# Kernel tuning notes

Measured on AMD Instinct MI355X. Metric: run time of the kernel, lower is better.

The kernel has to match this reference:

```python
import jax, jax.numpy as jnp
import numpy as np

H, W = 256, 832            # full-res organized point cloud (HEIGHT/WIDTH globals)
STRIDE_H, STRIDE_W = 2, 4  # stride_H_list[0], stride_W_list[0]
OUT_H, OUT_W = 128, 208    # out_H_list[0], out_W_list[0]
KH, KW = 12, 20            # layer0 kernel_size
K = 32                     # layer0 K_sample


def _sa_layer(pts, h_idx, w_idx, w1, b1, w2, b2, w3, b3):
    """PointNet SA: strided center selection, window KNN grouping, MLP, max-pool.
    pts: (B,H,W,3); h_idx/w_idx: (M,) full-res grid coords of selected centers.
    """
    B = pts.shape[0]
    pts_flat = pts.reshape(B, H * W, 3)
    center_idx = h_idx * W + w_idx                      # (M,)
    centers = pts_flat[:, center_idx]                   # (B,M,3)  fast_select gather
    # candidate window around each center (clipped at borders)
    dh = jnp.arange(KH) - KH // 2
    dw = jnp.arange(KW) - KW // 2
    cand_h = jnp.clip(h_idx[:, None] + dh, 0, H - 1)    # (M,KH)
    cand_w = jnp.clip(w_idx[:, None] + dw, 0, W - 1)    # (M,KW)
    cand_idx = (cand_h[:, :, None] * W + cand_w[:, None, :]).reshape(-1, KH * KW)  # (M,P)
    cand = pts_flat[:, cand_idx]                        # (B,M,P,3) irregular gather
    d2 = jnp.sum((cand - centers[:, :, None, :]) ** 2, axis=-1)  # (B,M,P)
    _, nn = jax.lax.top_k(-d2, K)                       # K nearest within window
    knn = jnp.take_along_axis(cand, nn[..., None], axis=2)       # (B,M,K,3)
    rel = knn - centers[:, :, None, :]                  # local coordinates
    h = jax.nn.relu(rel @ w1 + b1)                      # mlp [8,8,16]
    h = jax.nn.relu(h @ w2 + b2)
    h = jax.nn.relu(h @ w3 + b3)
    return centers, jnp.max(h, axis=2)                  # (B,M,3), (B,M,16)


def setup_inputs() -> dict:
    key = jax.random.key(0)
    ks = jax.random.split(key, 5)
    return {
        "pos1": jax.random.normal(ks[0], (2, H, W, 3), jnp.float32) * 5.0,
        "pos2": jax.random.normal(ks[1], (2, H, W, 3), jnp.float32) * 5.0,
        "w1": jax.random.normal(ks[2], (3, 8), jnp.float32) * 0.3,
        "b1": jnp.zeros((8,), jnp.float32),
        "w2": jax.random.normal(ks[3], (8, 8), jnp.float32) * 0.3,
        "b2": jnp.zeros((8,), jnp.float32),
        "w3": jax.random.normal(ks[4], (8, 16), jnp.float32) * 0.3,
        "b3": jnp.zeros((16,), jnp.float32),
    }


def reference(pos1, pos2, w1, b1, w2, b2, w3, b3):
    # get_selected_idx for level 0: strided grid subsampling
    h_idx = jnp.repeat(jnp.arange(OUT_H) * STRIDE_H, OUT_W)  # (M,)
    w_idx = jnp.tile(jnp.arange(OUT_W) * STRIDE_W, OUT_H)    # (M,)
    _, f1 = _sa_layer(pos1, h_idx, w_idx, w1, b1, w2, b2, w3, b3)
    _, f2 = _sa_layer(pos2, h_idx, w_idx, w1, b1, w2, b2, w3, b3)
    return jnp.concatenate([f1, f2], axis=-1)  # (B, OUT_H*OUT_W, 32)
```

## Files before the change

kernel.cpp:

```cpp
#include <hip/hip_runtime.h>
#include <hip/hip_bf16.h>

#define HH 256
#define WW 832
#define OHH 128
#define OWW 208
#define NCAND 240
#define MM (OHH*OWW)

__device__ __forceinline__ int iclamp(int v, int lo, int hi) { return min(max(v, lo), hi); }
__device__ __forceinline__ int mbcnt64(unsigned long long m) {
    return __builtin_amdgcn_mbcnt_hi((unsigned)(m >> 32),
           __builtin_amdgcn_mbcnt_lo((unsigned)(m & 0xFFFFFFFFull), 0));
}

__global__ void __launch_bounds__(256) sa_fused(
    const float* __restrict__ pos1, const float* __restrict__ pos2,
    const float* __restrict__ w1, const float* __restrict__ b1,
    const float* __restrict__ w2, const float* __restrict__ b2,
    const float* __restrict__ w3, const float* __restrict__ b3,
    float* __restrict__ out)
{
    __shared__ float4 sW1[8];
    __shared__ float4 sW2[8][2];
    __shared__ float4 sW3[16][2];
    __shared__ float  sB2v[8];
    __shared__ float  sB3v[16];
    __shared__ int    selJ[128];

    const int t = threadIdx.x;
    if (t < 8)  sW1[t] = make_float4(w1[t], w1[8 + t], w1[16 + t], b1[t]);
    if (t < 16) { int o = t >> 1, g = (t & 1) * 4;
        sW2[o][t & 1] = make_float4(w2[g*8 + o], w2[(g+1)*8 + o], w2[(g+2)*8 + o], w2[(g+3)*8 + o]); }
    if (t < 32) { int o = t >> 1, g = (t & 1) * 4;
        sW3[o][t & 1] = make_float4(w3[g*16 + o], w3[(g+1)*16 + o], w3[(g+2)*16 + o], w3[(g+3)*16 + o]); }
    if (t < 8)  sB2v[t] = b2[t];
    if (t < 16) sB3v[t] = b3[t];
    __syncthreads();

    const int lane = t & 63;
    const int wid  = t >> 6;
    const int m    = blockIdx.x * 4 + wid;
    const int b    = blockIdx.y & 1;
    const int cl   = blockIdx.y >> 1;
    const float* __restrict__ base = (cl ? pos2 : pos1) + (size_t)b * (HH * WW * 3);

    const unsigned um = (unsigned)m;
    const int oh = (int)(um / OWW);
    const int ow = (int)(um - (unsigned)oh * OWW);
    const int h0 = oh * 2, w0 = ow * 4;

    const float cx = base[(h0 * WW + w0) * 3 + 0];
    const float cy = base[(h0 * WW + w0) * 3 + 1];
    const float cz = base[(h0 * WW + w0) * 3 + 2];

    unsigned d2b[4];
    #pragma unroll
    for (int q = 0; q < 4; ++q) {
        int j  = q * 64 + lane;
        int kh = (j * 205) >> 12;
        int kw = j - kh * 20;
        int ch = iclamp(h0 - 6 + kh, 0, HH - 1);
        int cw = iclamp(w0 - 10 + kw, 0, WW - 1);
        const float* p = base + (ch * WW + cw) * 3;
        float dx = __fsub_rn(p[0], cx);
        float dy = __fsub_rn(p[1], cy);
        float dz = __fsub_rn(p[2], cz);
        float dd = __fadd_rn(__fadd_rn(__fmul_rn(dx, dx), __fmul_rn(dy, dy)), __fmul_rn(dz, dz));
        d2b[q] = (j < NCAND) ? __float_as_uint(dd) : 0xFFFFFFFFu;
    }

    unsigned T = 0;
    unsigned long long sm0 = 0, sm1 = 0, sm2 = 0, sm3 = 0;
    bool exact = false;
    for (int bpos = 30; bpos >= 0; --bpos) {
        unsigned Q = T | (1u << bpos);
        unsigned long long t0 = __ballot(d2b[0] < Q);
        unsigned long long t1 = __ballot(d2b[1] < Q);
        unsigned long long t2 = __ballot(d2b[2] < Q);
        unsigned long long t3 = __ballot(d2b[3] < Q);
        int c = __popcll(t0) + __popcll(t1) + __popcll(t2) + __popcll(t3);
        if (c == 32) { sm0 = t0; sm1 = t1; sm2 = t2; sm3 = t3; exact = true; break; }
        if (c < 32) T = Q;
    }
    if (!exact) {
        unsigned long long l0 = __ballot(d2b[0] < T);
        unsigned long long l1 = __ballot(d2b[1] < T);
        unsigned long long l2 = __ballot(d2b[2] < T);
        unsigned long long l3 = __ballot(d2b[3] < T);
        unsigned long long e0 = __ballot(d2b[0] == T);
        unsigned long long e1 = __ballot(d2b[1] == T);
        unsigned long long e2 = __ballot(d2b[2] == T);
        unsigned long long e3 = __ballot(d2b[3] == T);
        int c_lt = __popcll(l0) + __popcll(l1) + __popcll(l2) + __popcll(l3);
        int r = 32 - c_lt;
        int p1 = __popcll(e0), p2 = p1 + __popcll(e1), p3 = p2 + __popcll(e2);
        bool s0 = (d2b[0] < T) || ((d2b[0] == T) && (mbcnt64(e0) < r));
        bool s1 = (d2b[1] < T) || ((d2b[1] == T) && (p1 + mbcnt64(e1) < r));
        bool s2 = (d2b[2] < T) || ((d2b[2] == T) && (p2 + mbcnt64(e2) < r));
        bool s3 = (d2b[3] < T) || ((d2b[3] == T) && (p3 + mbcnt64(e3) < r));
        sm0 = __ballot(s0); sm1 = __ballot(s1); sm2 = __ballot(s2); sm3 = __ballot(s3);
    }

    {
        int b1 = __popcll(sm0);
        int b2 = b1 + __popcll(sm1);
        int b3 = b2 + __popcll(sm2);
        int lb = wid * 32;
        if ((sm0 >> lane) & 1) selJ[lb +      mbcnt64(sm0)] = lane;
        if ((sm1 >> lane) & 1) selJ[lb + b1 + mbcnt64(sm1)] = 64 + lane;
        if ((sm2 >> lane) & 1) selJ[lb + b2 + mbcnt64(sm2)] = 128 + lane;
        if ((sm3 >> lane) & 1) selJ[lb + b3 + mbcnt64(sm3)] = 192 + lane;
    }
    asm volatile("s_waitcnt lgkmcnt(0)" ::: "memory");
    __builtin_amdgcn_sched_barrier(0);

    {
        unsigned jj = (unsigned)selJ[wid * 32 + (lane & 31)];
        int kh = (int)((jj * 205u) >> 12);
        int kw = (int)jj - kh * 20;
        int ch = iclamp(h0 - 6 + kh, 0, HH - 1);
        int cw = iclamp(w0 - 10 + kw, 0, WW - 1);
        const float* p = base + (ch * WW + cw) * 3;
        float rx = __fsub_rn(p[0], cx);
        float ry = __fsub_rn(p[1], cy);
        float rz = __fsub_rn(p[2], cz);

        float h1[8];
        #pragma unroll
        for (int o = 0; o < 8; ++o) {
            float4 wv = sW1[o];
            h1[o] = fmaxf(fmaf(rz, wv.z, fmaf(ry, wv.y, fmaf(rx, wv.x, wv.w))), 0.f);
        }
        float h2[8];
        #pragma unroll
        for (int o = 0; o < 8; ++o) {
            float4 a = sW2[o][0], c4 = sW2[o][1];
            float v = sB2v[o];
            v = fmaf(h1[0], a.x, v);  v = fmaf(h1[1], a.y, v);
            v = fmaf(h1[2], a.z, v);  v = fmaf(h1[3], a.w, v);
            v = fmaf(h1[4], c4.x, v); v = fmaf(h1[5], c4.y, v);
            v = fmaf(h1[6], c4.z, v); v = fmaf(h1[7], c4.w, v);
            h2[o] = fmaxf(v, 0.f);
        }
        const int ob = (lane >> 5) << 3;
        float h3[8];
        #pragma unroll
        for (int o = 0; o < 8; ++o) {
            float4 a = sW3[ob + o][0], c4 = sW3[ob + o][1];
            float v = sB3v[ob + o];
            v = fmaf(h2[0], a.x, v);  v = fmaf(h2[1], a.y, v);
            v = fmaf(h2[2], a.z, v);  v = fmaf(h2[3], a.w, v);
            v = fmaf(h2[4], c4.x, v); v = fmaf(h2[5], c4.y, v);
            v = fmaf(h2[6], c4.z, v); v = fmaf(h2[7], c4.w, v);
            h3[o] = v;
        }
        #pragma unroll
        for (int o = 0; o < 8; ++o) {
            h3[o] = fmaxf(h3[o], __shfl_xor(h3[o], 16));
            h3[o] = fmaxf(h3[o], __shfl_xor(h3[o], 8));
            h3[o] = fmaxf(h3[o], __shfl_xor(h3[o], 4));
            h3[o] = fmaxf(h3[o], __shfl_xor(h3[o], 2));
            h3[o] = fmaxf(h3[o], __shfl_xor(h3[o], 1));
        }
        if ((lane & 31) == 0) {
            float4* dst = (float4*)(out + ((size_t)(b * MM + m) * 32) + (size_t)cl * 16 + ob);
            dst[0] = make_float4(fmaxf(h3[0], 0.f), fmaxf(h3[1], 0.f), fmaxf(h3[2], 0.f), fmaxf(h3[3], 0.f));
            dst[1] = make_float4(fmaxf(h3[4], 0.f), fmaxf(h3[5], 0.f), fmaxf(h3[6], 0.f), fmaxf(h3[7], 0.f));
        }
    }
}

extern "C" void kernel_launch(void* const* d_in, const int* in_sizes, int n_in,
                              void* d_out, int out_size, void* d_ws, size_t ws_size,
                              hipStream_t stream) {
    const float* pos1 = (const float*)d_in[0];
    const float* pos2 = (const float*)d_in[1];
    const float* w1   = (const float*)d_in[2];
    const float* b1   = (const float*)d_in[3];
    const float* w2   = (const float*)d_in[4];
    const float* b2   = (const float*)d_in[5];
    const float* w3   = (const float*)d_in[6];
    const float* b3   = (const float*)d_in[7];
    float* out = (float*)d_out;

    dim3 grid(MM / 4, 4);
    sa_fused<<<grid, 256, 0, stream>>>(pos1, pos2, w1, b1, w2, b2, w3, b3, out);
}
```

Baseline: 94.87 us.

## Stash selected relative coords in LDS and use packed FMA for MLP

The selected neighbours' relative xyz, already computed during the distance pass, are now written to shared memory. This replaces the index list that forced a second irregular global gather and index decode. The MLP layers are rewritten to use two-wide vector FMAs (packed fp32) with weights stored in pairs. The cost is more registers to hold dx/dy/dz for all candidates, and wider LDS writes (float4 instead of int).

New measurement: 95.53 us. About the same (+0.7%).

```diff
diff --git a/kernel.cpp b/kernel.cpp
--- a/kernel.cpp
+++ b/kernel.cpp
@@ -7,6 +7,8 @@
 #define OWW 208
 #define NCAND 240
 #define MM (OHH*OWW)
+
+typedef float v2f __attribute__((ext_vector_type(2)));
 
 __device__ __forceinline__ int iclamp(int v, int lo, int hi) { return min(max(v, lo), hi); }
 __device__ __forceinline__ int mbcnt64(unsigned long long m) {
@@ -21,21 +23,22 @@
     const float* __restrict__ w3, const float* __restrict__ b3,
     float* __restrict__ out)
 {
-    __shared__ float4 sW1[8];
-    __shared__ float4 sW2[8][2];
-    __shared__ float4 sW3[16][2];
-    __shared__ float  sB2v[8];
-    __shared__ float  sB3v[16];
-    __shared__ int    selJ[128];
+    __shared__ v2f sW1p[3][4];
+    __shared__ v2f sW2p[8][4];
+    __shared__ v2f sW3p[8][8];
+    __shared__ v2f sB1p[4], sB2p[4], sB3p[8];
+    __shared__ float4 selRel[128];
 
     const int t = threadIdx.x;
-    if (t < 8)  sW1[t] = make_float4(w1[t], w1[8 + t], w1[16 + t], b1[t]);
-    if (t < 16) { int o = t >> 1, g = (t & 1) * 4;
-        sW2[o][t & 1] = make_float4(w2[g*8 + o], w2[(g+1)*8 + o], w2[(g+2)*8 + o], w2[(g+3)*8 + o]); }
-    if (t < 32) { int o = t >> 1, g = (t & 1) * 4;
-        sW3[o][t & 1] = make_float4(w3[g*16 + o], w3[(g+1)*16 + o], w3[(g+2)*16 + o], w3[(g+3)*16 + o]); }
-    if (t < 8)  sB2v[t] = b2[t];
-    if (t < 16) sB3v[t] = b3[t];
+    if (t < 12)              { int i = t >> 2,  op = t & 3;
+        sW1p[i][op] = (v2f){w1[i*8 + 2*op], w1[i*8 + 2*op + 1]}; }
+    if (t >= 16 && t < 48)   { int u = t - 16, i = u >> 2, op = u & 3;
+        sW2p[i][op] = (v2f){w2[i*8 + 2*op], w2[i*8 + 2*op + 1]}; }
+    if (t >= 64 && t < 128)  { int u = t - 64, i = u >> 3, op = u & 7;
+        sW3p[i][op] = (v2f){w3[i*16 + 2*op], w3[i*16 + 2*op + 1]}; }
+    if (t >= 128 && t < 132) { int u = t - 128; sB1p[u] = (v2f){b1[2*u], b1[2*u + 1]}; }
+    if (t >= 132 && t < 136) { int u = t - 132; sB2p[u] = (v2f){b2[2*u], b2[2*u + 1]}; }
+    if (t >= 136 && t < 144) { int u = t - 136; sB3p[u] = (v2f){b3[2*u], b3[2*u + 1]}; }
     __syncthreads();
 
     const int lane = t & 63;
@@ -55,6 +58,7 @@
     const float cz = base[(h0 * WW + w0) * 3 + 2];
 
     unsigned d2b[4];
+    float dxv[4], dyv[4], dzv[4];
     #pragma unroll
     for (int q = 0; q < 4; ++q) {
         int j  = q * 64 + lane;
@@ -66,6 +70,7 @@
         float dx = __fsub_rn(p[0], cx);
         float dy = __fsub_rn(p[1], cy);
         float dz = __fsub_rn(p[2], cz);
+        dxv[q] = dx; dyv[q] = dy; dzv[q] = dz;
         float dd = __fadd_rn(__fadd_rn(__fmul_rn(dx, dx), __fmul_rn(dy, dy)), __fmul_rn(dz, dz));
         d2b[q] = (j < NCAND) ? __float_as_uint(dd) : 0xFFFFFFFFu;
     }
@@ -103,58 +108,63 @@
     }
 
     {
-        int b1 = __popcll(sm0);
-        int b2 = b1 + __popcll(sm1);
-        int b3 = b2 + __popcll(sm2);
+        int c1 = __popcll(sm0);
+        int c2 = c1 + __popcll(sm1);
+        int c3 = c2 + __popcll(sm2);
         int lb = wid * 32;
-        if ((sm0 >> lane) & 1) selJ[lb +      mbcnt64(sm0)] = lane;
-        if ((sm1 >> lane) & 1) selJ[lb + b1 + mbcnt64(sm1)] = 64 + lane;
-        if ((sm2 >> lane) & 1) selJ[lb + b2 + mbcnt64(sm2)] = 128 + lane;
-        if ((sm3 >> lane) & 1) selJ[lb + b3 + mbcnt64(sm3)] = 192 + lane;
+        if ((sm0 >> lane) & 1) selRel[lb +      mbcnt64(sm0)] = make_float4(dxv[0], dyv[0], dzv[0], 0.f);
+        if ((sm1 >> lane) & 1) selRel[lb + c1 + mbcnt64(sm1)] = make_float4(dxv[1], dyv[1], dzv[1], 0.f);
+        if ((sm2 >> lane) & 1) selRel[lb + c2 + mbcnt64(sm2)] = make_float4(dxv[2], dyv[2], dzv[2], 0.f);
+        if ((sm3 >> lane) & 1) selRel[lb + c3 + mbcnt64(sm3)] = make_float4(dxv[3], dyv[3], dzv[3], 0.f);
     }
     asm volatile("s_waitcnt lgkmcnt(0)" ::: "memory");
     __builtin_amdgcn_sched_barrier(0);
 
     {
-        unsigned jj = (unsigned)selJ[wid * 32 + (lane & 31)];
-        int kh = (int)((jj * 205u) >> 12);
-        int kw = (int)jj - kh * 20;
-        int ch = iclamp(h0 - 6 + kh, 0, HH - 1);
-        int cw = iclamp(w0 - 10 + kw, 0, WW - 1);
-        const float* p = base + (ch * WW + cw) * 3;
-        float rx = __fsub_rn(p[0], cx);
-        float ry = __fsub_rn(p[1], cy);
-        float rz = __fsub_rn(p[2], cz);
-
-        float h1[8];
-        #pragma unroll
-        for (int o = 0; o < 8; ++o) {
-            float4 wv = sW1[o];
-            h1[o] = fmaxf(fmaf(rz, wv.z, fmaf(ry, wv.y, fmaf(rx, wv.x, wv.w))), 0.f);
-        }
-        float h2[8];
-        #pragma unroll
-        for (int o = 0; o < 8; ++o) {
-            float4 a = sW2[o][0], c4 = sW2[o][1];
-            float v = sB2v[o];
-            v = fmaf(h1[0], a.x, v);  v = fmaf(h1[1], a.y, v);
-            v = fmaf(h1[2], a.z, v);  v = fmaf(h1[3], a.w, v);
-            v = fmaf(h1[4], c4.x, v); v = fmaf(h1[5], c4.y, v);
-            v = fmaf(h1[6], c4.z, v); v = fmaf(h1[7], c4.w, v);
-            h2[o] = fmaxf(v, 0.f);
-        }
-        const int ob = (lane >> 5) << 3;
+        float4 rel = selRel[wid * 32 + (lane & 31)];
+        v2f rx2 = (v2f){rel.x, rel.x};
+        v2f ry2 = (v2f){rel.y, rel.y};
+        v2f rz2 = (v2f){rel.z, rel.z};
+
+        v2f a1[4];
+        #pragma unroll
+        for (int op = 0; op < 4; ++op) {
+            v2f a = sB1p[op];
+            a = __builtin_elementwise_fma(rx2, sW1p[0][op], a);
+            a = __builtin_elementwise_fma(ry2, sW1p[1][op], a);
+            a = __builtin_elementwise_fma(rz2, sW1p[2][op], a);
+            a1[op] = __builtin_elementwise_max(a, (v2f)(0.f));
+        }
+        v2f a2[4];
+        #pragma unroll
+        for (int op = 0; op < 4; ++op) a2[op] = sB2p[op];
+        #pragma unroll
+        for (int i = 0; i < 8; ++i) {
+            float h = a1[i >> 1][i & 1];
+            v2f hb = (v2f){h, h};
+            #pragma unroll
+            for (int op = 0; op < 4; ++op)
+                a2[op] = __builtin_elementwise_fma(hb, sW2p[i][op], a2[op]);
+        }
+        #pragma unroll
+        for (int op = 0; op < 4; ++op) a2[op] = __builtin_elementwise_max(a2[op], (v2f)(0.f));
+
+        const int obp = (lane >> 5) << 2;
+        v2f a3[4];
+        #pragma unroll
+        for (int op = 0; op < 4; ++op) a3[op] = sB3p[obp + op];
+        #pragma unroll
+        for (int i = 0; i < 8; ++i) {
+            float h = a2[i >> 1][i & 1];
+            v2f hb = (v2f){h, h};
+            #pragma unroll
+            for (int op = 0; op < 4; ++op)
+                a3[op] = __builtin_elementwise_fma(hb, sW3p[i][obp + op], a3[op]);
+        }
         float h3[8];
         #pragma unroll
-        for (int o = 0; o < 8; ++o) {
-            float4 a = sW3[ob + o][0], c4 = sW3[ob + o][1];
-            float v = sB3v[ob + o];
-            v = fmaf(h2[0], a.x, v);  v = fmaf(h2[1], a.y, v);
-            v = fmaf(h2[2], a.z, v);  v = fmaf(h2[3], a.w, v);
-            v = fmaf(h2[4], c4.x, v); v = fmaf(h2[5], c4.y, v);
-            v = fmaf(h2[6], c4.z, v); v = fmaf(h2[7], c4.w, v);
-            h3[o] = v;
-        }
+        for (int o = 0; o < 8; ++o) h3[o] = a3[o >> 1][o & 1];
+
         #pragma unroll
         for (int o = 0; o < 8; ++o) {
             h3[o] = fmaxf(h3[o], __shfl_xor(h3[o], 16));
@@ -164,6 +174,7 @@
             h3[o] = fmaxf(h3[o], __shfl_xor(h3[o], 1));
         }
         if ((lane & 31) == 0) {
+            const int ob = (lane >> 5) << 3;
             float4* dst = (float4*)(out + ((size_t)(b * MM + m) * 32) + (size_t)cl * 16 + ob);
             dst[0] = make_float4(fmaxf(h3[0], 0.f), fmaxf(h3[1], 0.f), fmaxf(h3[2], 0.f), fmaxf(h3[3], 0.f));
             dst[1] = make_float4(fmaxf(h3[4], 0.f), fmaxf(h3[5], 0.f), fmaxf(h3[6], 0.f), fmaxf(h3[7], 0.f));
```
